# Optimization experiments

Measured on AMD Instinct MI355X. Metric: run time of the kernel, lower is better.

The kernel has to match this reference:

```python
import jax, jax.numpy as jnp
import numpy as np

N = 1_048_576  # rows
D = 64         # feature dim
OUTPUT_SHAPE = (N, D)


def setup_inputs() -> dict:
    key = jax.random.key(0)
    k1, k2, k3 = jax.random.split(key, 3)
    data = jax.random.normal(k1, (N, D), dtype=jnp.float32)
    # exactly balanced partition labels (N/2 zeros, N/2 ones), randomly interleaved
    partitions = jax.random.permutation(k2, jnp.arange(N, dtype=jnp.int32) % 2)
    # destination indices: a permutation of [0, N) split between the two partitions
    perm = jax.random.permutation(k3, jnp.arange(N, dtype=jnp.int32))
    index0 = perm[: N // 2]
    index1 = perm[N // 2 :]
    return {"data": data, "partitions": partitions, "index0": index0, "index1": index1}


def reference(data, partitions, index0, index1):
    # Fused dynamic_partition(num=2) + dynamic_stitch.
    # Row r with label p has rank = (# rows with label p among rows 0..r) - 1;
    # dynamic_partition preserves order, so its final destination is index_p[rank].
    is0 = partitions == 0
    rank0 = jnp.cumsum(is0.astype(jnp.int32)) - 1          # [N]
    rank1 = jnpp = jnp.cumsum((~is0).astype(jnp.int32)) - 1  # [N]
    n0 = index0.shape[0]
    n1 = index1.shape[0]
    dest0 = index0[jnp.clip(rank0, 0, n0 - 1)]             # [N]
    dest1 = index1[jnp.clip(rank1, 0, n1 - 1)]             # [N]
    oob = jnp.int32(OUTPUT_SHAPE[0])  # out-of-bounds sentinel, dropped by scatter
    # dynamic_stitch: later lists overwrite earlier ones on duplicate indices,
    # so scatter partition-0 rows first, then partition-1 rows.
    d0 = jnp.where(is0, dest0, oob)
    d1 = jnp.where(is0, oob, dest1)
    out = jnp.zeros(OUTPUT_SHAPE, data.dtype)
    out = out.at[d0].set(data, mode="drop")
    out = out.at[d1].set(data, mode="drop")
    return out
```

## Files before the change

kernel.cpp:

```cpp
#include <hip/hip_runtime.h>


#define BLOCK 256
#define F4_PER_ROW 16

typedef float f4 __attribute__((ext_vector_type(4)));

__global__ void count_zeros_kernel(const int* __restrict__ parts,
                                   int* __restrict__ blockCounts, int n) {
    int i = blockIdx.x * BLOCK + threadIdx.x;
    int is0 = (i < n && parts[i] == 0) ? 1 : 0;
    unsigned long long mask = __ballot(is0);
    __shared__ int wsum[BLOCK / 64];
    int lane = threadIdx.x & 63;
    int wave = threadIdx.x >> 6;
    if (lane == 0) wsum[wave] = __popcll(mask);
    __syncthreads();
    if (threadIdx.x == 0) {
        int s = 0;
        for (int w = 0; w < BLOCK / 64; ++w) s += wsum[w];
        blockCounts[blockIdx.x] = s;
    }
}

__global__ void scan_kernel(const int* __restrict__ blockCounts,
                            int* __restrict__ blockOffsets, int nb) {
    __shared__ int sums[256];
    int t = threadIdx.x;
    int per = (nb + 255) >> 8;
    if (per > 16) per = 16;
    int local[16];
    int s = 0;
    for (int j = 0; j < per; ++j) {
        int idx = t * per + j;
        int v = (idx < nb) ? blockCounts[idx] : 0;
        local[j] = s;
        s += v;
    }
    sums[t] = s;
    __syncthreads();
    for (int off = 1; off < 256; off <<= 1) {
        int add = (t >= off) ? sums[t - off] : 0;
        __syncthreads();
        sums[t] += add;
        __syncthreads();
    }
    int excl = (t > 0) ? sums[t - 1] : 0;
    for (int j = 0; j < per; ++j) {
        int idx = t * per + j;
        if (idx < nb) blockOffsets[idx] = excl + local[j];
    }
}

__global__ void build_inv_kernel(const int* __restrict__ parts,
                                 const int* __restrict__ idx0,
                                 const int* __restrict__ idx1,
                                 const int* __restrict__ blockZeroOff,
                                 int* __restrict__ inv,
                                 int n, int n0, int n1) {
    int i = blockIdx.x * BLOCK + threadIdx.x;
    int t = threadIdx.x;
    __shared__ int wzero[BLOCK / 64];

    int valid = (i < n) ? 1 : 0;
    int is0 = (valid && parts[i] == 0) ? 1 : 0;
    unsigned long long mask = __ballot(is0);
    int lane = t & 63;
    int wave = t >> 6;
    int zerosBeforeInWave = __popcll(mask & ((1ull << lane) - 1ull));
    if (lane == 63) wzero[wave] = zerosBeforeInWave + is0;
    __syncthreads();
    int waveOff = 0;
    for (int w = 0; w < wave; ++w) waveOff += wzero[w];
    int zerosBefore = blockZeroOff[blockIdx.x] + waveOff + zerosBeforeInWave;

    if (valid) {
        int d;
        if (is0) {
            int r = zerosBefore;
            if (r > n0 - 1) r = n0 - 1;
            d = idx0[r];
        } else {
            int r = i - zerosBefore;
            if (r > n1 - 1) r = n1 - 1;
            d = idx1[r];
        }
        if ((unsigned)d < (unsigned)n) inv[d] = i;
    }
}

__global__ void gather_kernel(const f4* __restrict__ data,
                              const int* __restrict__ inv,
                              f4* __restrict__ out, int n) {
    size_t total = (size_t)n * F4_PER_ROW;
    size_t stride = (size_t)gridDim.x * blockDim.x;
    size_t g = (size_t)blockIdx.x * blockDim.x + threadIdx.x;
#pragma unroll 8
    for (; g < total; g += stride) {
        int o = (int)(g >> 4);
        int l = (int)(g & 15);
        int s = inv[o];
        f4 v = data[(size_t)s * F4_PER_ROW + l];
        __builtin_nontemporal_store(v, &out[g]);
    }
}

extern "C" void kernel_launch(void* const* d_in, const int* in_sizes, int n_in,
                              void* d_out, int out_size, void* d_ws, size_t ws_size,
                              hipStream_t stream) {
    const float* data  = (const float*)d_in[0];
    const int*   parts = (const int*)d_in[1];
    const int*   idx0  = (const int*)d_in[2];
    const int*   idx1  = (const int*)d_in[3];
    float* out = (float*)d_out;

    int n  = in_sizes[1];
    int n0 = in_sizes[2];
    int n1 = in_sizes[3];

    int nb = (n + BLOCK - 1) / BLOCK;

    int* counts  = (int*)d_ws;
    int* offsets = counts + nb;
    int* inv     = offsets + nb;

    count_zeros_kernel<<<nb, BLOCK, 0, stream>>>(parts, counts, n);
    scan_kernel<<<1, 256, 0, stream>>>(counts, offsets, nb);
    build_inv_kernel<<<nb, BLOCK, 0, stream>>>(parts, idx0, idx1, offsets, inv, n, n0, n1);

    int gblocks = 8192;
    gather_kernel<<<gblocks, BLOCK, 0, stream>>>((const f4*)data, inv, (f4*)out, n);
}
```

Baseline: 486.1 us.

## Fuse inverse-index build and gather into a single direct scatter kernel

Replaces the two-step approach (build an inverse permutation array, then gather rows through it) with one kernel that computes each row's destination and scatters the row's 256 bytes directly to the output. This removes the inv array write and read and one kernel launch. Reads of data become fully coalesced while writes become scattered by whole rows. Rows whose destination is never written are no longer zero-filled, which only matters if the indices are not a full permutation.

Result: faster. 471.3 us (-3.0%).

```diff
diff --git a/kernel.cpp b/kernel.cpp
--- a/kernel.cpp
+++ b/kernel.cpp
@@ -52,15 +52,17 @@
     }
 }
 
-__global__ void build_inv_kernel(const int* __restrict__ parts,
-                                 const int* __restrict__ idx0,
-                                 const int* __restrict__ idx1,
-                                 const int* __restrict__ blockZeroOff,
-                                 int* __restrict__ inv,
-                                 int n, int n0, int n1) {
+__global__ void scatter_kernel(const f4* __restrict__ data,
+                               const int* __restrict__ parts,
+                               const int* __restrict__ idx0,
+                               const int* __restrict__ idx1,
+                               const int* __restrict__ blockZeroOff,
+                               f4* __restrict__ out,
+                               int n, int n0, int n1) {
     int i = blockIdx.x * BLOCK + threadIdx.x;
     int t = threadIdx.x;
     __shared__ int wzero[BLOCK / 64];
+    __shared__ int destS[BLOCK];
 
     int valid = (i < n) ? 1 : 0;
     int is0 = (valid && parts[i] == 0) ? 1 : 0;
@@ -74,8 +76,8 @@
     for (int w = 0; w < wave; ++w) waveOff += wzero[w];
     int zerosBefore = blockZeroOff[blockIdx.x] + waveOff + zerosBeforeInWave;
 
+    int d = n;
     if (valid) {
-        int d;
         if (is0) {
             int r = zerosBefore;
             if (r > n0 - 1) r = n0 - 1;
@@ -85,23 +87,26 @@
             if (r > n1 - 1) r = n1 - 1;
             d = idx1[r];
         }
-        if ((unsigned)d < (unsigned)n) inv[d] = i;
     }
-}
+    destS[t] = d;
+    __syncthreads();
 
-__global__ void gather_kernel(const f4* __restrict__ data,
-                              const int* __restrict__ inv,
-                              f4* __restrict__ out, int n) {
-    size_t total = (size_t)n * F4_PER_ROW;
-    size_t stride = (size_t)gridDim.x * blockDim.x;
-    size_t g = (size_t)blockIdx.x * blockDim.x + threadIdx.x;
-#pragma unroll 8
-    for (; g < total; g += stride) {
-        int o = (int)(g >> 4);
-        int l = (int)(g & 15);
-        int s = inv[o];
-        f4 v = data[(size_t)s * F4_PER_ROW + l];
-        __builtin_nontemporal_store(v, &out[g]);
+    size_t srcBase = (size_t)blockIdx.x * BLOCK * F4_PER_ROW;
+
+    f4 v[F4_PER_ROW];
+    int dd[F4_PER_ROW];
+#pragma unroll
+    for (int j = 0; j < F4_PER_ROW; ++j) {
+        int f = j * BLOCK + t;
+        dd[j] = destS[f >> 4];
+        if ((unsigned)dd[j] < (unsigned)n) v[j] = data[srcBase + f];
+    }
+#pragma unroll
+    for (int j = 0; j < F4_PER_ROW; ++j) {
+        int f = j * BLOCK + t;
+        int l = f & 15;
+        if ((unsigned)dd[j] < (unsigned)n)
+            __builtin_nontemporal_store(v[j], &out[(size_t)dd[j] * F4_PER_ROW + l]);
     }
 }
 
@@ -122,12 +127,9 @@
 
     int* counts  = (int*)d_ws;
     int* offsets = counts + nb;
-    int* inv     = offsets + nb;
 
     count_zeros_kernel<<<nb, BLOCK, 0, stream>>>(parts, counts, n);
     scan_kernel<<<1, 256, 0, stream>>>(counts, offsets, nb);
-    build_inv_kernel<<<nb, BLOCK, 0, stream>>>(parts, idx0, idx1, offsets, inv, n, n0, n1);
-
-    int gblocks = 8192;
-    gather_kernel<<<gblocks, BLOCK, 0, stream>>>((const f4*)data, inv, (f4*)out, n);
+    scatter_kernel<<<nb, BLOCK, 0, stream>>>((const f4*)data, parts, idx0, idx1,
+                                             offsets, (f4*)out, n, n0, n1);
 }
```
